# Kernel optimization log

Hardware: AMD Instinct MI355X
Metric: run time of the kernel (lower is better)

The kernel has to match this reference:

```python
import jax, jax.numpy as jnp
import numpy as np

N_NODES = 50000
N_EDGES = 400000
D = 64          # in_feats == out_feats (transform=False)
DIST_DIM = 32
NUM = 5         # num_neighbor
N_BOUND = 64    # embedding table rows = N_BOUND + 1


def setup_inputs() -> dict:
    key = jax.random.key(0)
    ks = jax.random.split(key, 9)
    feat = jax.random.normal(ks[0], (N_NODES, D), dtype=jnp.float32)
    loc = jax.random.uniform(ks[1], (N_NODES, 2), dtype=jnp.float32)
    embed_table = jax.random.normal(ks[2], (N_BOUND + 1, DIST_DIM), dtype=jnp.float32)
    G_w = jax.random.normal(ks[3], (D, DIST_DIM), dtype=jnp.float32) / np.sqrt(DIST_DIM)
    agg_w = jax.random.normal(ks[4], (D, 2 * D), dtype=jnp.float32) / np.sqrt(2 * D)
    agg_b = jnp.zeros((D,), dtype=jnp.float32)
    boundaries = jnp.linspace(0.0, 2.0, N_BOUND).astype(jnp.float32)
    src = jax.random.randint(ks[5], (N_EDGES,), 0, N_NODES, dtype=jnp.int32)
    dst = jax.random.randint(ks[6], (N_EDGES,), 0, N_NODES, dtype=jnp.int32)
    inter_ids = jax.random.randint(ks[7], (N_EDGES, NUM), 0, N_NODES, dtype=jnp.int32)
    return {"feat": feat, "loc": loc, "embed_table": embed_table, "G_w": G_w,
            "agg_w": agg_w, "agg_b": agg_b, "boundaries": boundaries,
            "src": src, "dst": dst, "inter_ids": inter_ids}


def reference(feat, loc, embed_table, G_w, agg_w, agg_b, boundaries, src, dst, inter_ids):
    n = feat.shape[0]
    e, num = inter_ids.shape
    one = jnp.ones((e,), dtype=jnp.float32)
    # degrees: d0 = in_deg^-0.5 (at dst), d2 = out_deg^-0.5 (at src), clamp(min=1)
    in_deg = jnp.maximum(jax.ops.segment_sum(one, dst, num_segments=n), 1.0)
    out_deg = jnp.maximum(jax.ops.segment_sum(one, src, num_segments=n), 1.0)
    d0 = in_deg ** -0.5  # [N]
    d2 = out_deg ** -0.5  # [N]
    # dist1: dst->src node distance per edge
    loc_src = loc[src]                                   # [E,2]
    dist1 = jnp.linalg.norm(loc[dst] - loc_src, axis=1)  # [E]
    # dist_: src to each sampled intermediate node
    inter_pos = loc[inter_ids]                                     # [E,num,2]
    dist_ = jnp.linalg.norm(loc_src[:, None, :] - inter_pos, axis=-1)  # [E,num]
    # bucketize (torch right=False == searchsorted side='left') -> embed -> linear G
    b1 = jnp.searchsorted(boundaries, dist1, side='left')   # [E]
    b_ = jnp.searchsorted(boundaries, dist_, side='left')   # [E,num]
    dist_embed1 = embed_table[b1] @ G_w.T                    # [E,D]
    dist_embed_ = embed_table[b_] @ G_w.T                    # [E,num,D]
    # mean over sampled intermediates of (dist-embed * gathered feat)
    dist_embed_dot_h = (dist_embed_ * feat[inter_ids]).mean(axis=1)  # [E,D]
    # agg_fc on concat, degree-scaled
    cat = jnp.concatenate([dist_embed1 * feat[src], dist_embed_dot_h], axis=1)  # [E,2D]
    h = (d0[dst] * d2[src])[:, None] * (cat @ agg_w.T + agg_b)                  # [E,D]
    # copy_e / sum: scatter-sum edges to dst nodes
    rst = jax.ops.segment_sum(h, dst, num_segments=n)  # [N,D]
    return rst
```

## Files before the change

### kernel.cpp

```cpp
#include <hip/hip_runtime.h>


#define DFEAT 64

typedef __attribute__((ext_vector_type(8))) _Float16 half8;
typedef __attribute__((ext_vector_type(4))) float floatx4;

__device__ __forceinline__ void sb8d(int2 q, float (&f)[8]) {
#pragma unroll
    for (int t = 0; t < 4; ++t) f[t] = (float)((q.x << (24 - 8 * t)) >> 24);
#pragma unroll
    for (int t = 0; t < 4; ++t) f[4 + t] = (float)((q.y << (24 - 8 * t)) >> 24);
}

__device__ __forceinline__ int bucketize(float x, float bnd) {
    int i = (int)(x * 31.5f);
    i = min(max(i, 0), 64);
#pragma unroll
    for (int t = 0; t < 3; ++t) {
        float bi = __shfl(bnd, min(i, 63));
        if (i < 64 && bi < x) ++i;
    }
#pragma unroll
    for (int t = 0; t < 2; ++t) {
        float bim = __shfl(bnd, max(i - 1, 0));
        if (i > 0 && bim >= x) --i;
    }
    return i;
}

__global__ void k_prep(const float* __restrict__ Etab,
                       const float* __restrict__ G, float* __restrict__ P,
                       float* __restrict__ rst, float* __restrict__ degs,
                       const float* __restrict__ feat,
                       signed char* __restrict__ featQ,
                       float* __restrict__ scaleQ, int nRst, int nDeg) {
    int i = blockIdx.x * blockDim.x + threadIdx.x;
    if (i < nDeg) degs[i] = 0.0f;
    if (i < 65 * DFEAT) {
        int b = i >> 6, o = i & 63;
        float a = 0.0f;
#pragma unroll
        for (int m = 0; m < 32; ++m)
            a = fmaf(Etab[b * 32 + m], G[o * 32 + m], a);
        P[i] = a;
    }
    if (i < nRst) {
        rst[i] = 0.0f;
        if (featQ) {
            float f = feat[i];
            float a = fabsf(f);
#pragma unroll
            for (int o = 32; o; o >>= 1) a = fmaxf(a, __shfl_xor(a, o));
            float inv = (a > 0.0f) ? 127.0f / a : 0.0f;
            featQ[i] = (signed char)__float2int_rn(f * inv);
            if ((i & 63) == 0) scaleQ[i >> 6] = a * (1.0f / 127.0f);
        }
    }
}

__global__ void k_deg(const int* __restrict__ src, const int* __restrict__ dst,
                      float* __restrict__ degs, int N, int E) {
    int i = blockIdx.x * blockDim.x + threadIdx.x;
    if (i < E) {
        atomicAdd(&degs[dst[i]], 1.0f);
        atomicAdd(&degs[N + src[i]], 1.0f);
    }
}

#define PPAD 68

__global__ __launch_bounds__(256, 4) void k_edge(
    const float* __restrict__ feat, const signed char* __restrict__ featQ,
    const float* __restrict__ scaleQ, const float* __restrict__ loc,
    const float* __restrict__ agg_w, const float* __restrict__ agg_b,
    const float* __restrict__ bnds, const int* __restrict__ src,
    const int* __restrict__ dst, const int* __restrict__ inter,
    const float* __restrict__ P, const float* __restrict__ degs,
    float* __restrict__ rst, int N, int E) {
    const int tid = threadIdx.x;
    const int lane = tid & 63;
    const int wid = tid >> 6;
    const int m16 = lane & 15;
    const int quad = lane >> 4;

    __shared__ float sP[65 * PPAD];
    __shared__ half8 sWB[16 * 64];

    for (int i = tid; i < 65 * DFEAT; i += 256)
        sP[(i >> 6) * PPAD + (i & 63)] = P[i];

    for (int f = wid; f < 16; f += 4) {
        int sl = f >> 2, nt = f & 3;
        const float* wp = agg_w + (nt * 16 + m16) * 128 + sl * 32 + quad * 8;
        floatx4 wa = *(const floatx4*)wp;
        floatx4 wb = *(const floatx4*)(wp + 4);
        float xs[8] = {wa.x, wa.y, wa.z, wa.w, wb.x, wb.y, wb.z, wb.w};
        half8 h;
#pragma unroll
        for (int j = 0; j < 8; ++j) h[j] = (_Float16)xs[j];
        sWB[f * 64 + lane] = h;
    }

    const float bnd = bnds[lane];
    float bias4[4];
#pragma unroll
    for (int nt = 0; nt < 4; ++nt) bias4[nt] = agg_b[nt * 16 + m16];

    __syncthreads();

    const int nstream = gridDim.x << 2;
    const int wstream = (blockIdx.x << 2) + wid;
    const int ngroups = (E + 15) >> 4;
    const bool haveQ = (featQ != nullptr);
    const int k0q = quad * 8;

    for (int g = wstream; g < ngroups; g += nstream) {
        const int em = (g << 4) + m16;
        const bool act = em < E;
        const int ec = act ? em : 0;

        const int s = __builtin_nontemporal_load(src + ec);
        const int d = __builtin_nontemporal_load(dst + ec);
        int ij[5];
#pragma unroll
        for (int j = 0; j < 5; ++j)
            ij[j] = __builtin_nontemporal_load(inter + ec * 5 + j);

        const float2 ls = ((const float2*)loc)[s];
        const float2 ld = ((const float2*)loc)[d];
        float2 lj[5];
#pragma unroll
        for (int j = 0; j < 5; ++j) lj[j] = ((const float2*)loc)[ij[j]];
        const float dgd = degs[d];
        const float dgs = degs[N + s];

        half8 A[4];
        float dsc;
        int b1;
        if (haveQ) {
            const float ssrc = scaleQ[s];
            float sq[5];
#pragma unroll
            for (int j = 0; j < 5; ++j) sq[j] = scaleQ[ij[j]];

            const signed char* qrow = featQ + (s << 6);
            int2 qu[2];
            qu[0] = *(const int2*)(qrow + k0q);
            qu[1] = *(const int2*)(qrow + 32 + k0q);
            int2 qv[2][5];
#pragma unroll
            for (int sl = 0; sl < 2; ++sl)
#pragma unroll
                for (int j = 0; j < 5; ++j)
                    qv[sl][j] =
                        *(const int2*)(featQ + (ij[j] << 6) + sl * 32 + k0q);

            dsc = rsqrtf(fmaxf(dgd, 1.0f)) * rsqrtf(fmaxf(dgs, 1.0f));
            if (!act) dsc = 0.0f;
            float dx = ld.x - ls.x, dy = ld.y - ls.y;
            b1 = bucketize(sqrtf(dx * dx + dy * dy), bnd);
            int bj[5];
#pragma unroll
            for (int j = 0; j < 5; ++j) {
                float ex = ls.x - lj[j].x, ey = ls.y - lj[j].y;
                bj[j] = bucketize(sqrtf(ex * ex + ey * ey), bnd);
            }

            const float* prow = sP + b1 * PPAD;
#pragma unroll
            for (int sl = 0; sl < 2; ++sl) {
                int k0 = sl * 32 + k0q;
                float fq[8];
                sb8d(qu[sl], fq);
                floatx4 pa = *(const floatx4*)(prow + k0);
                floatx4 pb = *(const floatx4*)(prow + k0 + 4);
                float xs[8] = {fq[0] * ssrc * pa.x, fq[1] * ssrc * pa.y,
                               fq[2] * ssrc * pa.z, fq[3] * ssrc * pa.w,
                               fq[4] * ssrc * pb.x, fq[5] * ssrc * pb.y,
                               fq[6] * ssrc * pb.z, fq[7] * ssrc * pb.w};
                half8 h;
#pragma unroll
                for (int j = 0; j < 8; ++j) h[j] = (_Float16)xs[j];
                A[sl] = h;
            }
#pragma unroll
            for (int sl = 0; sl < 2; ++sl) {
                int k0 = sl * 32 + k0q;
                float r[8] = {0, 0, 0, 0, 0, 0, 0, 0};
#pragma unroll
                for (int j = 0; j < 5; ++j) {
                    float fq[8];
                    sb8d(qv[sl][j], fq);
                    const float sj = sq[j];
                    const float* pr = sP + bj[j] * PPAD;
                    floatx4 pa = *(const floatx4*)(pr + k0);
                    floatx4 pb = *(const floatx4*)(pr + k0 + 4);
                    r[0] = fmaf(fq[0] * sj, pa.x, r[0]);
                    r[1] = fmaf(fq[1] * sj, pa.y, r[1]);
                    r[2] = fmaf(fq[2] * sj, pa.z, r[2]);
                    r[3] = fmaf(fq[3] * sj, pa.w, r[3]);
                    r[4] = fmaf(fq[4] * sj, pb.x, r[4]);
                    r[5] = fmaf(fq[5] * sj, pb.y, r[5]);
                    r[6] = fmaf(fq[6] * sj, pb.z, r[6]);
                    r[7] = fmaf(fq[7] * sj, pb.w, r[7]);
                }
                half8 h;
#pragma unroll
                for (int j = 0; j < 8; ++j) h[j] = (_Float16)(r[j] * 0.2f);
                A[2 + sl] = h;
            }
        } else {
            dsc = rsqrtf(fmaxf(dgd, 1.0f)) * rsqrtf(fmaxf(dgs, 1.0f));
            if (!act) dsc = 0.0f;
            float dx = ld.x - ls.x, dy = ld.y - ls.y;
            b1 = bucketize(sqrtf(dx * dx + dy * dy), bnd);
            int bj[5];
#pragma unroll
            for (int j = 0; j < 5; ++j) {
                float ex = ls.x - lj[j].x, ey = ls.y - lj[j].y;
                bj[j] = bucketize(sqrtf(ex * ex + ey * ey), bnd);
            }
            const float* frow = feat + (s << 6);
            const float* prow = sP + b1 * PPAD;
#pragma unroll
            for (int sl = 0; sl < 2; ++sl) {
                int k0 = sl * 32 + k0q;
                floatx4 fa = *(const floatx4*)(frow + k0);
                floatx4 fb = *(const floatx4*)(frow + k0 + 4);
                floatx4 pa = *(const floatx4*)(prow + k0);
                floatx4 pb = *(const floatx4*)(prow + k0 + 4);
                float xs[8] = {fa.x * pa.x, fa.y * pa.y, fa.z * pa.z,
                               fa.w * pa.w, fb.x * pb.x, fb.y * pb.y,
                               fb.z * pb.z, fb.w * pb.w};
                half8 h;
#pragma unroll
                for (int j = 0; j < 8; ++j) h[j] = (_Float16)xs[j];
                A[sl] = h;
            }
#pragma unroll
            for (int sl = 0; sl < 2; ++sl) {
                int k0 = sl * 32 + k0q;
                float r[8] = {0, 0, 0, 0, 0, 0, 0, 0};
#pragma unroll
                for (int j = 0; j < 5; ++j) {
                    const float* fr = feat + (ij[j] << 6);
                    const float* pr = sP + bj[j] * PPAD;
                    floatx4 fa = *(const floatx4*)(fr + k0);
                    floatx4 fb = *(const floatx4*)(fr + k0 + 4);
                    floatx4 pa = *(const floatx4*)(pr + k0);
                    floatx4 pb = *(const floatx4*)(pr + k0 + 4);
                    r[0] = fmaf(fa.x, pa.x, r[0]);
                    r[1] = fmaf(fa.y, pa.y, r[1]);
                    r[2] = fmaf(fa.z, pa.z, r[2]);
                    r[3] = fmaf(fa.w, pa.w, r[3]);
                    r[4] = fmaf(fb.x, pb.x, r[4]);
                    r[5] = fmaf(fb.y, pb.y, r[5]);
                    r[6] = fmaf(fb.z, pb.z, r[6]);
                    r[7] = fmaf(fb.w, pb.w, r[7]);
                }
                half8 h;
#pragma unroll
                for (int j = 0; j < 8; ++j) h[j] = (_Float16)(r[j] * 0.2f);
                A[2 + sl] = h;
            }
        }

        floatx4 acc[4] = {{0, 0, 0, 0}, {0, 0, 0, 0}, {0, 0, 0, 0}, {0, 0, 0, 0}};
#pragma unroll
        for (int sl = 0; sl < 4; ++sl) {
#pragma unroll
            for (int nt = 0; nt < 4; ++nt) {
                half8 b = sWB[((sl << 2) + nt) * 64 + lane];
                acc[nt] = __builtin_amdgcn_mfma_f32_16x16x32_f16(
                    A[sl], b, acc[nt], 0, 0, 0);
            }
        }

#pragma unroll
        for (int r = 0; r < 4; ++r) {
            const int m = (quad << 2) + r;
            const int dm = __shfl(d, m);
            const float sc = __shfl(dsc, m);
            float* ap = rst + (dm << 6) + m16;
            float v0 = (acc[0][r] + bias4[0]) * sc;
            float v1 = (acc[1][r] + bias4[1]) * sc;
            float v2 = (acc[2][r] + bias4[2]) * sc;
            float v3 = (acc[3][r] + bias4[3]) * sc;
            asm volatile("global_atomic_add_f32 %0, %1, off nt"
                         :: "v"(ap), "v"(v0));
            asm volatile("global_atomic_add_f32 %0, %1, off offset:64 nt"
                         :: "v"(ap), "v"(v1));
            asm volatile("global_atomic_add_f32 %0, %1, off offset:128 nt"
                         :: "v"(ap), "v"(v2));
            asm volatile("global_atomic_add_f32 %0, %1, off offset:192 nt"
                         :: "v"(ap), "v"(v3));
        }
    }
}

extern "C" void kernel_launch(void* const* d_in, const int* in_sizes, int n_in,
                              void* d_out, int out_size, void* d_ws,
                              size_t ws_size, hipStream_t stream) {
    const float* feat  = (const float*)d_in[0];
    const float* loc   = (const float*)d_in[1];
    const float* embed = (const float*)d_in[2];
    const float* G_w   = (const float*)d_in[3];
    const float* agg_w = (const float*)d_in[4];
    const float* agg_b = (const float*)d_in[5];
    const float* bnds  = (const float*)d_in[6];
    const int* src   = (const int*)d_in[7];
    const int* dst   = (const int*)d_in[8];
    const int* inter = (const int*)d_in[9];

    const int N = in_sizes[0] / DFEAT;
    const int E = in_sizes[7];

    float* rst = (float*)d_out;
    float* ws = (float*)d_ws;
    float* degs = ws;
    float* P = ws + 2 * (size_t)N;
    float* scaleQ = P + 65 * DFEAT;

    size_t fixed_bytes = (2 * (size_t)N + 65 * DFEAT + (size_t)N) * sizeof(float);
    size_t fq_off = (fixed_bytes + 15) & ~(size_t)15;
    size_t need = fq_off + (size_t)N * DFEAT;
    signed char* featQ =
        (ws_size >= need) ? (signed char*)((char*)d_ws + fq_off) : nullptr;

    const int nRst = N * DFEAT;
    const int nDeg = 2 * N;

    k_prep<<<(nRst + 255) / 256, 256, 0, stream>>>(
        embed, G_w, P, rst, degs, feat, featQ, scaleQ, nRst, nDeg);
    k_deg<<<(E + 255) / 256, 256, 0, stream>>>(src, dst, degs, N, E);
    k_edge<<<1024, 256, 0, stream>>>(feat, featQ, scaleQ, loc, agg_w, agg_b,
                                     bnds, src, dst, inter, P, degs, rst, N, E);
}
```

Before: 262.7 us.

## Bucket edges by destination and pre-combine same-destination rows before atomic scatter

```diff
diff --git a/kernel.cpp b/kernel.cpp
--- a/kernel.cpp
+++ b/kernel.cpp
@@ -65,6 +65,46 @@
     if (i < E) {
         atomicAdd(&degs[dst[i]], 1.0f);
         atomicAdd(&degs[N + src[i]], 1.0f);
+    }
+}
+
+__global__ void k_scan(const float* __restrict__ degs, int* __restrict__ binptr,
+                       int N) {
+    __shared__ int part[256];
+    int t = threadIdx.x;
+    int chunk = (N + 255) >> 8;
+    int lo = t * chunk, hi = min(lo + chunk, N);
+    int s = 0;
+    for (int i = lo; i < hi; ++i) s += (int)degs[i];
+    part[t] = s;
+    __syncthreads();
+    if (t == 0) {
+        int run = 0;
+        for (int i = 0; i < 256; ++i) { int v = part[i]; part[i] = run; run += v; }
+    }
+    __syncthreads();
+    int run = part[t];
+    for (int i = lo; i < hi; ++i) {
+        int c = (int)degs[i];
+        binptr[i] = run;
+        run += c;
+    }
+}
+
+__global__ void k_scatter(const int* __restrict__ src,
+                          const int* __restrict__ dst,
+                          const int* __restrict__ inter,
+                          int* __restrict__ binptr, int* __restrict__ srcS,
+                          int* __restrict__ dstS, int* __restrict__ interS,
+                          int E) {
+    int i = blockIdx.x * blockDim.x + threadIdx.x;
+    if (i < E) {
+        int dd = dst[i];
+        int pos = atomicAdd(&binptr[dd], 1);
+        dstS[pos] = dd;
+        srcS[pos] = src[i];
+#pragma unroll
+        for (int j = 0; j < 5; ++j) interS[pos * 5 + j] = inter[i * 5 + j];
     }
 }
 
@@ -109,13 +149,17 @@
 
     __syncthreads();
 
-    const int nstream = gridDim.x << 2;
-    const int wstream = (blockIdx.x << 2) + wid;
+    const int nw = gridDim.x << 2;
+    const int wi = (blockIdx.x << 2) + wid;
     const int ngroups = (E + 15) >> 4;
     const bool haveQ = (featQ != nullptr);
     const int k0q = quad * 8;
 
-    for (int g = wstream; g < ngroups; g += nstream) {
+    const int qq = ngroups / nw, rr = ngroups - qq * nw;
+    const int g0 = wi * qq + min(wi, rr);
+    const int g1 = g0 + qq + (wi < rr ? 1 : 0);
+
+    for (int g = g0; g < g1; ++g) {
         const int em = (g << 4) + m16;
         const bool act = em < E;
         const int ec = act ? em : 0;
@@ -277,24 +321,77 @@
             }
         }
 
-#pragma unroll
-        for (int r = 0; r < 4; ++r) {
-            const int m = (quad << 2) + r;
-            const int dm = __shfl(d, m);
-            const float sc = __shfl(dsc, m);
-            float* ap = rst + (dm << 6) + m16;
-            float v0 = (acc[0][r] + bias4[0]) * sc;
-            float v1 = (acc[1][r] + bias4[1]) * sc;
-            float v2 = (acc[2][r] + bias4[2]) * sc;
-            float v3 = (acc[3][r] + bias4[3]) * sc;
-            asm volatile("global_atomic_add_f32 %0, %1, off nt"
-                         :: "v"(ap), "v"(v0));
-            asm volatile("global_atomic_add_f32 %0, %1, off offset:64 nt"
-                         :: "v"(ap), "v"(v1));
-            asm volatile("global_atomic_add_f32 %0, %1, off offset:128 nt"
-                         :: "v"(ap), "v"(v2));
-            asm volatile("global_atomic_add_f32 %0, %1, off offset:192 nt"
-                         :: "v"(ap), "v"(v3));
+        const int q4 = quad << 2;
+        const int dm0 = __shfl(d, q4 + 0), dm1 = __shfl(d, q4 + 1);
+        const int dm2 = __shfl(d, q4 + 2), dm3 = __shfl(d, q4 + 3);
+        const float sc0 = __shfl(dsc, q4 + 0), sc1 = __shfl(dsc, q4 + 1);
+        const float sc2 = __shfl(dsc, q4 + 2), sc3 = __shfl(dsc, q4 + 3);
+        const int dmn = __shfl(d, (q4 + 4) & 15);
+        const int dmp = __shfl(d, (q4 - 1) & 15);
+        const bool eq0 = dm0 == dm1, eq1 = dm1 == dm2, eq2 = dm2 == dm3;
+        const bool eq3 = (quad < 3) && (dm3 == dmn);
+        const bool lnk = (quad > 0) && (dmp == dm0);
+        const bool alls = eq0 && eq1 && eq2;
+        const bool gate = alls && lnk;
+
+        float w0[4], w1[4], w2[4], w3[4], Ci[4];
+#pragma unroll
+        for (int nt = 0; nt < 4; ++nt) {
+            w0[nt] = (acc[nt][0] + bias4[nt]) * sc0;
+            w1[nt] = (acc[nt][1] + bias4[nt]) * sc1;
+            w2[nt] = (acc[nt][2] + bias4[nt]) * sc2;
+            w3[nt] = (acc[nt][3] + bias4[nt]) * sc3;
+            if (eq0) w1[nt] += w0[nt];
+            if (eq1) w2[nt] += w1[nt];
+            if (eq2) w3[nt] += w2[nt];
+            float T = w3[nt];
+#pragma unroll
+            for (int k = 0; k < 3; ++k) {
+                float Tp = __shfl(T, (lane - 16) & 63);
+                T = w3[nt] + (gate ? Tp : 0.0f);
+            }
+            float c = __shfl(T, (lane - 16) & 63);
+            Ci[nt] = lnk ? c : 0.0f;
+        }
+
+        if (!eq0) {
+            float* ap = rst + (dm0 << 6) + m16;
+            float v0 = w0[0] + Ci[0], v1 = w0[1] + Ci[1];
+            float v2 = w0[2] + Ci[2], v3 = w0[3] + Ci[3];
+            asm volatile("global_atomic_add_f32 %0, %1, off nt" :: "v"(ap), "v"(v0));
+            asm volatile("global_atomic_add_f32 %0, %1, off offset:64 nt" :: "v"(ap), "v"(v1));
+            asm volatile("global_atomic_add_f32 %0, %1, off offset:128 nt" :: "v"(ap), "v"(v2));
+            asm volatile("global_atomic_add_f32 %0, %1, off offset:192 nt" :: "v"(ap), "v"(v3));
+        }
+        if (!eq1) {
+            float* ap = rst + (dm1 << 6) + m16;
+            float h0 = eq0 ? Ci[0] : 0.0f, h1 = eq0 ? Ci[1] : 0.0f;
+            float h2 = eq0 ? Ci[2] : 0.0f, h3 = eq0 ? Ci[3] : 0.0f;
+            float v0 = w1[0] + h0, v1 = w1[1] + h1;
+            float v2 = w1[2] + h2, v3 = w1[3] + h3;
+            asm volatile("global_atomic_add_f32 %0, %1, off nt" :: "v"(ap), "v"(v0));
+            asm volatile("global_atomic_add_f32 %0, %1, off offset:64 nt" :: "v"(ap), "v"(v1));
+            asm volatile("global_atomic_add_f32 %0, %1, off offset:128 nt" :: "v"(ap), "v"(v2));
+            asm volatile("global_atomic_add_f32 %0, %1, off offset:192 nt" :: "v"(ap), "v"(v3));
+        }
+        if (!eq2) {
+            const bool hr = eq0 && eq1;
+            float* ap = rst + (dm2 << 6) + m16;
+            float v0 = w2[0] + (hr ? Ci[0] : 0.0f), v1 = w2[1] + (hr ? Ci[1] : 0.0f);
+            float v2 = w2[2] + (hr ? Ci[2] : 0.0f), v3 = w2[3] + (hr ? Ci[3] : 0.0f);
+            asm volatile("global_atomic_add_f32 %0, %1, off nt" :: "v"(ap), "v"(v0));
+            asm volatile("global_atomic_add_f32 %0, %1, off offset:64 nt" :: "v"(ap), "v"(v1));
+            asm volatile("global_atomic_add_f32 %0, %1, off offset:128 nt" :: "v"(ap), "v"(v2));
+            asm volatile("global_atomic_add_f32 %0, %1, off offset:192 nt" :: "v"(ap), "v"(v3));
+        }
+        if (!eq3) {
+            float* ap = rst + (dm3 << 6) + m16;
+            float v0 = w3[0] + (alls ? Ci[0] : 0.0f), v1 = w3[1] + (alls ? Ci[1] : 0.0f);
+            float v2 = w3[2] + (alls ? Ci[2] : 0.0f), v3 = w3[3] + (alls ? Ci[3] : 0.0f);
+            asm volatile("global_atomic_add_f32 %0, %1, off nt" :: "v"(ap), "v"(v0));
+            asm volatile("global_atomic_add_f32 %0, %1, off offset:64 nt" :: "v"(ap), "v"(v1));
+            asm volatile("global_atomic_add_f32 %0, %1, off offset:128 nt" :: "v"(ap), "v"(v2));
+            asm volatile("global_atomic_add_f32 %0, %1, off offset:192 nt" :: "v"(ap), "v"(v3));
         }
     }
 }
@@ -324,9 +421,22 @@
 
     size_t fixed_bytes = (2 * (size_t)N + 65 * DFEAT + (size_t)N) * sizeof(float);
     size_t fq_off = (fixed_bytes + 15) & ~(size_t)15;
-    size_t need = fq_off + (size_t)N * DFEAT;
+    size_t need_q = fq_off + (size_t)N * DFEAT;
     signed char* featQ =
-        (ws_size >= need) ? (signed char*)((char*)d_ws + fq_off) : nullptr;
+        (ws_size >= need_q) ? (signed char*)((char*)d_ws + fq_off) : nullptr;
+
+    size_t so = (need_q + 15) & ~(size_t)15;
+    size_t need_sort = so + ((size_t)N + 7 * (size_t)E) * sizeof(int);
+    int* binptr = nullptr;
+    int* srcS = nullptr;
+    int* dstS = nullptr;
+    int* interS = nullptr;
+    if (ws_size >= need_sort) {
+        binptr = (int*)((char*)d_ws + so);
+        srcS = binptr + N;
+        dstS = srcS + E;
+        interS = dstS + E;
+    }
 
     const int nRst = N * DFEAT;
     const int nDeg = 2 * N;
@@ -334,6 +444,18 @@
     k_prep<<<(nRst + 255) / 256, 256, 0, stream>>>(
         embed, G_w, P, rst, degs, feat, featQ, scaleQ, nRst, nDeg);
     k_deg<<<(E + 255) / 256, 256, 0, stream>>>(src, dst, degs, N, E);
+    const int* srcE = src;
+    const int* dstE = dst;
+    const int* interE = inter;
+    if (binptr) {
+        k_scan<<<1, 256, 0, stream>>>(degs, binptr, N);
+        k_scatter<<<(E + 255) / 256, 256, 0, stream>>>(
+            src, dst, inter, binptr, srcS, dstS, interS, E);
+        srcE = srcS;
+        dstE = dstS;
+        interE = interS;
+    }
     k_edge<<<1024, 256, 0, stream>>>(feat, featQ, scaleQ, loc, agg_w, agg_b,
-                                     bnds, src, dst, inter, P, degs, rst, N, E);
-}
+                                     bnds, srcE, dstE, interE, P, degs, rst,
+                                     N, E);
+}
```

Result: slower. 327.3 us (+24.6%).
